# Performance work log

Measured on AMD Instinct MI355X. Metric: run time of the kernel, lower is better.

Reference implementation:

```python
import jax, jax.numpy as jnp
import numpy as np

I, O, R = 64, 64, 896          # input / output / regulatory protein counts
N = I + O + R                  # total GRN size
WARMUP = 25                    # warmup_count


def setup_inputs() -> dict:
    key = jax.random.key(0)
    k1, k2, k3, k4 = jax.random.split(key, 4)
    return {
        "inputs": jax.random.uniform(k1, (16384, I), dtype=jnp.float32),
        "identifiers": jax.random.uniform(k2, (N,), dtype=jnp.float32),
        "enhancers": jax.random.uniform(k3, (N,), dtype=jnp.float32),
        "inhibitors": jax.random.uniform(k4, (N,), dtype=jnp.float32),
        "beta": jnp.full((1,), 2.0, dtype=jnp.float32),
        "delta": jnp.full((1,), 1.0, dtype=jnp.float32),
    }


def _signatures(identifiers, enhancers, inhibitors, beta):
    # sig[j, i] = exp(-beta * |tag_j - id_i|): affinity of protein j regulating protein i.
    enh = jnp.exp(-beta * jnp.abs(enhancers[:, None] - identifiers[None, :]))
    inh = jnp.exp(-beta * jnp.abs(inhibitors[:, None] - identifiers[None, :]))
    # output proteins do not regulate others -> zero their rows
    mask = jnp.ones((N,), dtype=enh.dtype).at[I:I + O].set(0.0)[:, None]
    return enh * mask, inh * mask


def _step(conc, sig_diff, delta):
    # conc: [..., N]; sig_diff = enh_sigs - inh_sigs: [N, N]
    dc = (delta / N) * (conc @ sig_diff)
    new = jnp.maximum(conc + dc, 0.0)
    reg = new[..., I:]                                    # outputs + regulatory
    s = jnp.sum(reg, axis=-1, keepdims=True)
    reg = jnp.where(s > 0, reg / s, reg)                  # renormalize
    return jnp.concatenate([conc[..., :I], reg], axis=-1)  # inputs clamped


def reference(inputs, identifiers, enhancers, inhibitors, beta, delta):
    b, d = beta[0], delta[0]
    enh_s, inh_s = _signatures(identifiers, enhancers, inhibitors, b)
    sig_diff = enh_s - inh_s

    # setup(): uniform initial concentrations; warmup(): shared sequential steps
    conc0 = jnp.full((N,), 1.0 / N, dtype=jnp.float32)
    def warm(c, _):
        return _step(c, sig_diff, d), None
    conc, _ = jax.lax.scan(warm, conc0, None, length=WARMUP)

    # per-sample (batched instead of tf.map_fn): set input concs, one step
    B = inputs.shape[0]
    batch_conc = jnp.concatenate(
        [inputs, jnp.broadcast_to(conc[I:], (B, N - I))], axis=-1)
    new = _step(batch_conc, sig_diff, d)
    return new[..., I:I + O]  # output protein concentrations [B, O]
```

## Files before the change

### kernel.cpp

```cpp
#include <hip/hip_runtime.h>
#include <math.h>

#define NJ 960
#define NWARM 25
#define NFB 64
#define NC 15

typedef unsigned long long u64;
typedef unsigned int u32;

#define WK_F   4096u
#define BASE_F (WK_F + 64u * 960u)

__device__ __forceinline__ u64 pack_tv(u32 tag, float v) {
  return ((u64)tag << 32) | (u64)__float_as_uint(v);
}
__device__ __forceinline__ void ast(u64* p, u64 v) {
  __hip_atomic_store(p, v, __ATOMIC_RELAXED, __HIP_MEMORY_SCOPE_AGENT);
}
__device__ __forceinline__ u64 ald(const u64* p) {
  return __hip_atomic_load(p, __ATOMIC_RELAXED, __HIP_MEMORY_SCOPE_AGENT);
}

__global__ __launch_bounds__(1024) void front_k(const float* __restrict__ ident,
                                                const float* __restrict__ enh,
                                                const float* __restrict__ inh,
                                                const float* __restrict__ beta,
                                                const float* __restrict__ delta,
                                                void* __restrict__ wsv) {
  u64* Y = (u64*)wsv;
  u64* P = Y + 2 * NJ;
  float* Wk = (float*)wsv + WK_F;
  float* base = (float*)wsv + BASE_F;

  __shared__ float S2loc[NC * NJ];
  __shared__ float yloc[NJ];
  __shared__ float pvals[NFB];
  __shared__ float psums[NC];
  __shared__ float hdl[NC];

  const int tid = threadIdx.x;
  const int wid = tid >> 6, lane = tid & 63;
  const int b = blockIdx.x;
  const int j0 = b * NC;
  const float bc = beta[0];
  const float dN = delta[0] / 1024.0f;

  if (wid < NC) {
    int j = j0 + wid;
    float cj = ident[64 + j];
    float wv = dN * (expf(-bc * fabsf(enh[lane] - cj)) -
                     expf(-bc * fabsf(inh[lane] - cj)));
    Wk[(size_t)lane * NJ + j] = wv;
    float h = wv;
    #pragma unroll
    for (int off = 32; off >= 1; off >>= 1) h += __shfl_xor(h, off);
    if (lane == 0) hdl[wid] = h * (1.0f / 1024.0f);
  }
  for (int idx = tid; idx < NC * NJ; idx += 1024) {
    int c = idx / NJ, m = idx - c * NJ;
    float v = 0.0f;
    if (m >= 64) {
      float cj = ident[64 + j0 + c];
      int g = 64 + m;
      v = dN * (expf(-bc * fabsf(enh[g] - cj)) - expf(-bc * fabsf(inh[g] - cj)));
    }
    S2loc[idx] = v;
  }
  if (tid < NC) ast(&Y[j0 + tid], pack_tv(1u, 1.0f / 1024.0f));
  __syncthreads();

  for (int t = 0; t <= NWARM; ++t) {
    if (tid < NJ) {
      u64* src = &Y[(size_t)(t & 1) * NJ + tid];
      u64 v = ald(src);
      while ((u32)(v >> 32) != (u32)(t + 1)) {
        __builtin_amdgcn_s_sleep(1);
        v = ald(src);
      }
      yloc[tid] = __uint_as_float((u32)v);
    }
    if (t > 0 && tid < NFB) {
      u64* src = &P[(size_t)(t & 1) * NFB + tid];
      u64 v = ald(src);
      while ((u32)(v >> 32) != (u32)(t + 1)) {
        __builtin_amdgcn_s_sleep(1);
        v = ald(src);
      }
      pvals[tid] = __uint_as_float((u32)v);
    }
    __syncthreads();

    float s = 1.0f;
    if (t > 0) {
      float acc = 0.0f;
      #pragma unroll
      for (int i = 0; i < NFB; ++i) acc += pvals[i];
      s = acc;
    }

    if (wid < NC) {
      const float* __restrict__ row = &S2loc[wid * NJ];
      float d = 0.0f;
      #pragma unroll
      for (int i = 0; i < 15; ++i)
        d = fmaf(yloc[lane + 64 * i], row[lane + 64 * i], d);
      #pragma unroll
      for (int off = 32; off >= 1; off >>= 1) d += __shfl_xor(d, off);
      if (lane == 0) {
        float pre = yloc[j0 + wid] + d;
        pre = (s > 0.0f) ? pre / s : pre;
        if (t < NWARM) {
          float yv = fmaxf(pre + hdl[wid], 0.0f);
          psums[wid] = yv;
          ast(&Y[(size_t)((t + 1) & 1) * NJ + j0 + wid],
              pack_tv((u32)(t + 2), yv));
        } else {
          base[j0 + wid] = pre;
        }
      }
    }
    __syncthreads();

    if (t < NWARM && tid < NFB) {
      float pv = (tid < NC) ? psums[tid] : 0.0f;
      #pragma unroll
      for (int off = 32; off >= 1; off >>= 1) pv += __shfl_xor(pv, off);
      if (tid == 0)
        ast(&P[(size_t)((t + 1) & 1) * NFB + b], pack_tv((u32)(t + 2), pv));
    }
  }
}

__global__ __launch_bounds__(512) void batch_t(const float* __restrict__ inp,
                                               const float* __restrict__ ws,
                                               float* __restrict__ out) {
  __shared__ float At[64][66];
  __shared__ float Wl[16][516];
  __shared__ float bch[512];

  const int tid = threadIdx.x;
  const int colg = tid & 63;
  const int rowg = tid >> 6;
  const size_t rowbase = (size_t)blockIdx.x * 64;
  const float* __restrict__ Wk = ws + WK_F;
  const float* __restrict__ base = ws + BASE_F;

  #pragma unroll
  for (int i = 0; i < 2; ++i) {
    int fi = tid + i * 512;
    int r = fi >> 4, c4 = (fi & 15) * 4;
    float4 f4 = *(const float4*)(inp + (rowbase + r) * 64 + c4);
    At[c4 + 0][r] = f4.x; At[c4 + 1][r] = f4.y;
    At[c4 + 2][r] = f4.z; At[c4 + 3][r] = f4.w;
  }

  float rs[8];
  #pragma unroll
  for (int r = 0; r < 8; ++r) rs[r] = 0.0f;
  float acc[8][8];

  #pragma unroll 1
  for (int ch = 0; ch < 2; ++ch) {
    const int c0 = ch ? 0 : 512;
    #pragma unroll
    for (int r = 0; r < 8; ++r)
      #pragma unroll
      for (int c = 0; c < 8; ++c) acc[r][c] = 0.0f;

    __syncthreads();
    {
      int j = c0 + tid;
      bch[tid] = (j < 960) ? base[j] : -1.0e30f;
    }

    #pragma unroll 1
    for (int s = 0; s < 4; ++s) {
      __syncthreads();
      #pragma unroll
      for (int i = 0; i < 4; ++i) {
        int fi = tid + i * 512;
        int kk = fi >> 7;
        int c4 = (fi & 127) * 4;
        int j = c0 + c4;
        float4 v = make_float4(0.f, 0.f, 0.f, 0.f);
        if (j < 960)
          v = *(const float4*)(Wk + (size_t)(16 * s + kk) * NJ + j);
        *(float4*)&Wl[kk][c4] = v;
      }
      __syncthreads();

      #pragma unroll
      for (int kk = 0; kk < 16; ++kk) {
        float4 a0 = *(const float4*)&At[16 * s + kk][rowg * 8];
        float4 a1 = *(const float4*)&At[16 * s + kk][rowg * 8 + 4];
        float4 w0 = *(const float4*)&Wl[kk][colg * 8];
        float4 w1 = *(const float4*)&Wl[kk][colg * 8 + 4];
        float a[8] = {a0.x, a0.y, a0.z, a0.w, a1.x, a1.y, a1.z, a1.w};
        float w[8] = {w0.x, w0.y, w0.z, w0.w, w1.x, w1.y, w1.z, w1.w};
        #pragma unroll
        for (int r = 0; r < 8; ++r)
          #pragma unroll
          for (int c = 0; c < 8; ++c)
            acc[r][c] = fmaf(a[r], w[c], acc[r][c]);
      }
    }

    #pragma unroll
    for (int c = 0; c < 8; ++c) {
      float bv = bch[colg * 8 + c];
      #pragma unroll
      for (int r = 0; r < 8; ++r)
        rs[r] += fmaxf(acc[r][c] + bv, 0.0f);
    }
  }

  #pragma unroll
  for (int r = 0; r < 8; ++r) {
    float v = rs[r];
    #pragma unroll
    for (int off = 32; off >= 1; off >>= 1) v += __shfl_xor(v, off);
    rs[r] = v;
  }

  if (colg < 8) {
    #pragma unroll
    for (int r = 0; r < 8; ++r) {
      float inv = (rs[r] > 0.0f) ? 1.0f / rs[r] : 1.0f;
      float* op = out + (rowbase + rowg * 8 + r) * 64 + colg * 8;
      float4 o;
      o.x = fmaxf(acc[r][0] + bch[colg * 8 + 0], 0.0f) * inv;
      o.y = fmaxf(acc[r][1] + bch[colg * 8 + 1], 0.0f) * inv;
      o.z = fmaxf(acc[r][2] + bch[colg * 8 + 2], 0.0f) * inv;
      o.w = fmaxf(acc[r][3] + bch[colg * 8 + 3], 0.0f) * inv;
      *(float4*)op = o;
      o.x = fmaxf(acc[r][4] + bch[colg * 8 + 4], 0.0f) * inv;
      o.y = fmaxf(acc[r][5] + bch[colg * 8 + 5], 0.0f) * inv;
      o.z = fmaxf(acc[r][6] + bch[colg * 8 + 6], 0.0f) * inv;
      o.w = fmaxf(acc[r][7] + bch[colg * 8 + 7], 0.0f) * inv;
      *(float4*)(op + 4) = o;
    }
  }
}

extern "C" void kernel_launch(void* const* d_in, const int* in_sizes, int n_in,
                              void* d_out, int out_size, void* d_ws, size_t ws_size,
                              hipStream_t stream) {
  const float* inp   = (const float*)d_in[0];
  const float* ident = (const float*)d_in[1];
  const float* enh   = (const float*)d_in[2];
  const float* inh   = (const float*)d_in[3];
  const float* beta  = (const float*)d_in[4];
  const float* delta = (const float*)d_in[5];

  hipLaunchKernelGGL(front_k, dim3(NFB), dim3(1024), 0, stream,
                     ident, enh, inh, beta, delta, d_ws);
  hipLaunchKernelGGL(batch_t, dim3(256), dim3(512), 0, stream,
                     inp, (const float*)d_ws, (float*)d_out);
}
```

Baseline: 181.7 us.

## Replace warmup matvec with sorted prefix-sum evaluation of exp-abs kernel in one block

The warmup recurrence now runs in a single block. Each step's dense 960x896 matvec is replaced by an algebraic split: exp(-b|x-c|) factors into exp(±b x)·exp(∓b c), so the sums come from prefix scans over sources sorted by enhancer and inhibitor tags. Helper blocks compute the ranks, counts, the input-protein contributions and the W matrix, and publish them through tagged atomic flags. This removes the 64-block cross-block spin barriers on every step, at the cost of numerical risk from exp(b*x) products and a single-block serial chain.

```diff
diff --git a/kernel.cpp b/kernel.cpp
--- a/kernel.cpp
+++ b/kernel.cpp
@@ -2,133 +2,242 @@
 #include <math.h>
 
 #define NJ 960
+#define NSRC 896
 #define NWARM 25
-#define NFB 64
-#define NC 15
 
 typedef unsigned long long u64;
 typedef unsigned int u32;
 
-#define WK_F   4096u
+#define RK_O   0u
+#define CT_O   896u
+#define HD_O   1856u
+#define WK_F   8192u
 #define BASE_F (WK_F + 64u * 960u)
 
-__device__ __forceinline__ u64 pack_tv(u32 tag, float v) {
-  return ((u64)tag << 32) | (u64)__float_as_uint(v);
-}
+#define TAG_RK 0x524B0001u
+#define TAG_CT 0x43540001u
+#define TAG_HD 0x48440001u
+
 __device__ __forceinline__ void ast(u64* p, u64 v) {
   __hip_atomic_store(p, v, __ATOMIC_RELAXED, __HIP_MEMORY_SCOPE_AGENT);
 }
 __device__ __forceinline__ u64 ald(const u64* p) {
   return __hip_atomic_load(p, __ATOMIC_RELAXED, __HIP_MEMORY_SCOPE_AGENT);
 }
-
-__global__ __launch_bounds__(1024) void front_k(const float* __restrict__ ident,
-                                                const float* __restrict__ enh,
-                                                const float* __restrict__ inh,
-                                                const float* __restrict__ beta,
-                                                const float* __restrict__ delta,
-                                                void* __restrict__ wsv) {
-  u64* Y = (u64*)wsv;
-  u64* P = Y + 2 * NJ;
+__device__ __forceinline__ u32 poll32(const u64* p, u32 tag) {
+  u64 v = ald(p);
+  while ((u32)(v >> 32) != tag) { __builtin_amdgcn_s_sleep(1); v = ald(p); }
+  return (u32)v;
+}
+
+__global__ __launch_bounds__(256) void front_k(const float* __restrict__ ident,
+                                               const float* __restrict__ enh,
+                                               const float* __restrict__ inh,
+                                               const float* __restrict__ beta,
+                                               const float* __restrict__ delta,
+                                               void* __restrict__ wsv) {
+  u64* RK = (u64*)wsv + RK_O;
+  u64* CT = (u64*)wsv + CT_O;
+  u64* HD = (u64*)wsv + HD_O;
   float* Wk = (float*)wsv + WK_F;
   float* base = (float*)wsv + BASE_F;
 
-  __shared__ float S2loc[NC * NJ];
-  __shared__ float yloc[NJ];
-  __shared__ float pvals[NFB];
-  __shared__ float psums[NC];
-  __shared__ float hdl[NC];
-
   const int tid = threadIdx.x;
-  const int wid = tid >> 6, lane = tid & 63;
-  const int b = blockIdx.x;
-  const int j0 = b * NC;
-  const float bc = beta[0];
+  const float bb = beta[0];
   const float dN = delta[0] / 1024.0f;
 
-  if (wid < NC) {
-    int j = j0 + wid;
-    float cj = ident[64 + j];
-    float wv = dN * (expf(-bc * fabsf(enh[lane] - cj)) -
-                     expf(-bc * fabsf(inh[lane] - cj)));
-    Wk[(size_t)lane * NJ + j] = wv;
-    float h = wv;
-    #pragma unroll
-    for (int off = 32; off >= 1; off >>= 1) h += __shfl_xor(h, off);
-    if (lane == 0) hdl[wid] = h * (1.0f / 1024.0f);
-  }
-  for (int idx = tid; idx < NC * NJ; idx += 1024) {
-    int c = idx / NJ, m = idx - c * NJ;
-    float v = 0.0f;
-    if (m >= 64) {
-      float cj = ident[64 + j0 + c];
-      int g = 64 + m;
-      v = dN * (expf(-bc * fabsf(enh[g] - cj)) - expf(-bc * fabsf(inh[g] - cj)));
-    }
-    S2loc[idx] = v;
-  }
-  if (tid < NC) ast(&Y[j0 + tid], pack_tv(1u, 1.0f / 1024.0f));
+  if (blockIdx.x > 0) {
+    const int g = (blockIdx.x - 1) * 256 + tid;
+    const int c8 = g & 7;
+    if (g < NSRC * 8) {
+      int m = g >> 3;
+      float myE = enh[128 + m], myI = inh[128 + m];
+      int re = 0, ri = 0;
+      for (int i = 112 * c8; i < 112 * c8 + 112; ++i) {
+        float ev = enh[128 + i], iv = inh[128 + i];
+        re += (ev < myE || (ev == myE && i < m)) ? 1 : 0;
+        ri += (iv < myI || (iv == myI && i < m)) ? 1 : 0;
+      }
+      int p = re | (ri << 16);
+      p += __shfl_xor(p, 1); p += __shfl_xor(p, 2); p += __shfl_xor(p, 4);
+      if (c8 == 0) ast(&RK[m], ((u64)TAG_RK << 32) | (u32)p);
+    }
+    {
+      int j = g >> 3;
+      float cj = ident[64 + j];
+      int ce = 0, ci = 0;
+      for (int i = 112 * c8; i < 112 * c8 + 112; ++i) {
+        ce += (enh[128 + i] <= cj) ? 1 : 0;
+        ci += (inh[128 + i] <= cj) ? 1 : 0;
+      }
+      int p = ce | (ci << 16);
+      p += __shfl_xor(p, 1); p += __shfl_xor(p, 2); p += __shfl_xor(p, 4);
+      if (c8 == 0) ast(&CT[j], ((u64)TAG_CT << 32) | (u32)p);
+    }
+    {
+      int j = g >> 3;
+      float cj = ident[64 + j];
+      float h = 0.0f;
+      for (int k = 8 * c8; k < 8 * c8 + 8; ++k)
+        h += expf(-bb * fabsf(enh[k] - cj)) - expf(-bb * fabsf(inh[k] - cj));
+      h += __shfl_xor(h, 1); h += __shfl_xor(h, 2); h += __shfl_xor(h, 4);
+      if (c8 == 0)
+        ast(&HD[j], ((u64)TAG_HD << 32) |
+                    (u64)__float_as_uint(dN * h * (1.0f / 1024.0f)));
+    }
+    {
+      int k = g / 120;
+      int jb = (g % 120) * 8;
+      float ek = enh[k], ik = inh[k];
+      #pragma unroll
+      for (int u = 0; u < 8; ++u) {
+        float cj = ident[64 + jb + u];
+        Wk[(size_t)k * NJ + jb + u] =
+            dN * (expf(-bb * fabsf(ek - cj)) - expf(-bb * fabsf(ik - cj)));
+      }
+    }
+    return;
+  }
+
+  __shared__ float yl[NJ];
+  __shared__ float2 scanE[1024];
+  __shared__ float2 scanI[1024];
+  __shared__ float4 wtot[4];
+  __shared__ float ssw[4];
+
+  const int lane = tid & 63, wvid = tid >> 6;
+
+  int rE[4], rI[4];
+  if (tid < 224) {
+    #pragma unroll
+    for (int s = 0; s < 4; ++s) {
+      u32 v = poll32(&RK[4 * tid + s], TAG_RK);
+      rE[s] = v & 0xFFFF; rI[s] = v >> 16;
+    }
+  }
+  int cE[4], cI[4];
+  float hd[4], fm[4], fp[4];
+  if (tid < 240) {
+    #pragma unroll
+    for (int c = 0; c < 4; ++c) {
+      u32 v = poll32(&CT[4 * tid + c], TAG_CT);
+      cE[c] = v & 0xFFFF; cI[c] = v >> 16;
+      hd[c] = __uint_as_float(poll32(&HD[4 * tid + c], TAG_HD));
+      float cj = ident[64 + 4 * tid + c];
+      fm[c] = expf(-bb * cj); fp[c] = expf(bb * cj);
+    }
+  }
+  float EP[4], EN[4], IP[4], IN2[4];
+  if (tid < 224) {
+    #pragma unroll
+    for (int s = 0; s < 4; ++s) {
+      float e = enh[128 + 4 * tid + s], i2 = inh[128 + 4 * tid + s];
+      EP[s] = expf(bb * e);  EN[s] = expf(-bb * e);
+      IP[s] = expf(bb * i2); IN2[s] = expf(-bb * i2);
+    }
+  }
+  float y_own[4] = {1.0f / 1024.0f, 1.0f / 1024.0f, 1.0f / 1024.0f, 1.0f / 1024.0f};
+  if (tid < 240) {
+    #pragma unroll
+    for (int c = 0; c < 4; ++c) yl[4 * tid + c] = 1.0f / 1024.0f;
+  }
   __syncthreads();
 
   for (int t = 0; t <= NWARM; ++t) {
-    if (tid < NJ) {
-      u64* src = &Y[(size_t)(t & 1) * NJ + tid];
-      u64 v = ald(src);
-      while ((u32)(v >> 32) != (u32)(t + 1)) {
-        __builtin_amdgcn_s_sleep(1);
-        v = ald(src);
-      }
-      yloc[tid] = __uint_as_float((u32)v);
-    }
-    if (t > 0 && tid < NFB) {
-      u64* src = &P[(size_t)(t & 1) * NFB + tid];
-      u64 v = ald(src);
-      while ((u32)(v >> 32) != (u32)(t + 1)) {
-        __builtin_amdgcn_s_sleep(1);
-        v = ald(src);
-      }
-      pvals[tid] = __uint_as_float((u32)v);
-    }
-    __syncthreads();
-
-    float s = 1.0f;
-    if (t > 0) {
-      float acc = 0.0f;
-      #pragma unroll
-      for (int i = 0; i < NFB; ++i) acc += pvals[i];
-      s = acc;
-    }
-
-    if (wid < NC) {
-      const float* __restrict__ row = &S2loc[wid * NJ];
-      float d = 0.0f;
-      #pragma unroll
-      for (int i = 0; i < 15; ++i)
-        d = fmaf(yloc[lane + 64 * i], row[lane + 64 * i], d);
-      #pragma unroll
-      for (int off = 32; off >= 1; off >>= 1) d += __shfl_xor(d, off);
-      if (lane == 0) {
-        float pre = yloc[j0 + wid] + d;
-        pre = (s > 0.0f) ? pre / s : pre;
+    if (tid == 0) {
+      scanE[0] = make_float2(0.f, 0.f);
+      scanI[0] = make_float2(0.f, 0.f);
+    }
+    if (tid >= 224) {
+      #pragma unroll
+      for (int c = 0; c < 4; ++c) {
+        int p = 4 * tid + c;
+        if (p > NSRC) {
+          scanE[p] = make_float2(0.f, 0.f);
+          scanI[p] = make_float2(0.f, 0.f);
+        }
+      }
+    }
+    if (tid < 224) {
+      #pragma unroll
+      for (int s = 0; s < 4; ++s) {
+        float ym = yl[64 + 4 * tid + s];
+        scanE[rE[s] + 1] = make_float2(ym * EP[s], ym * EN[s]);
+        scanI[rI[s] + 1] = make_float2(ym * IP[s], ym * IN2[s]);
+      }
+    }
+    __syncthreads();
+
+    float2 e0 = scanE[4 * tid], e1 = scanE[4 * tid + 1],
+           e2 = scanE[4 * tid + 2], e3 = scanE[4 * tid + 3];
+    float2 i0 = scanI[4 * tid], i1 = scanI[4 * tid + 1],
+           i2v = scanI[4 * tid + 2], i3 = scanI[4 * tid + 3];
+    e1.x += e0.x; e1.y += e0.y; e2.x += e1.x; e2.y += e1.y; e3.x += e2.x; e3.y += e2.y;
+    i1.x += i0.x; i1.y += i0.y; i2v.x += i1.x; i2v.y += i1.y; i3.x += i2v.x; i3.y += i2v.y;
+    float4 tot = make_float4(e3.x, e3.y, i3.x, i3.y);
+    float4 inc = tot;
+    #pragma unroll
+    for (int off = 1; off < 64; off <<= 1) {
+      float ox = __shfl_up(inc.x, off, 64);
+      float oy = __shfl_up(inc.y, off, 64);
+      float oz = __shfl_up(inc.z, off, 64);
+      float ow = __shfl_up(inc.w, off, 64);
+      if (lane >= off) { inc.x += ox; inc.y += oy; inc.z += oz; inc.w += ow; }
+    }
+    if (lane == 63) wtot[wvid] = inc;
+    __syncthreads();
+    float4 exc = make_float4(inc.x - tot.x, inc.y - tot.y,
+                             inc.z - tot.z, inc.w - tot.w);
+    #pragma unroll
+    for (int w = 0; w < 3; ++w)
+      if (w < wvid) {
+        float4 p = wtot[w];
+        exc.x += p.x; exc.y += p.y; exc.z += p.z; exc.w += p.w;
+      }
+    e0.x += exc.x; e0.y += exc.y; e1.x += exc.x; e1.y += exc.y;
+    e2.x += exc.x; e2.y += exc.y; e3.x += exc.x; e3.y += exc.y;
+    i0.x += exc.z; i0.y += exc.w; i1.x += exc.z; i1.y += exc.w;
+    i2v.x += exc.z; i2v.y += exc.w; i3.x += exc.z; i3.y += exc.w;
+    scanE[4 * tid] = e0; scanE[4 * tid + 1] = e1;
+    scanE[4 * tid + 2] = e2; scanE[4 * tid + 3] = e3;
+    scanI[4 * tid] = i0; scanI[4 * tid + 1] = i1;
+    scanI[4 * tid + 2] = i2v; scanI[4 * tid + 3] = i3;
+    __syncthreads();
+
+    float nv[4] = {0.f, 0.f, 0.f, 0.f};
+    float psum = 0.0f;
+    if (tid < 240) {
+      float2 TE = scanE[NSRC], TI = scanI[NSRC];
+      #pragma unroll
+      for (int c = 0; c < 4; ++c) {
+        float2 AE = scanE[cE[c]], AI = scanI[cI[c]];
+        float dot = fm[c] * AE.x + fp[c] * (TE.y - AE.y)
+                  - fm[c] * AI.x - fp[c] * (TI.y - AI.y);
+        float pre = y_own[c] + dN * dot;
         if (t < NWARM) {
-          float yv = fmaxf(pre + hdl[wid], 0.0f);
-          psums[wid] = yv;
-          ast(&Y[(size_t)((t + 1) & 1) * NJ + j0 + wid],
-              pack_tv((u32)(t + 2), yv));
+          nv[c] = fmaxf(pre + hd[c], 0.0f);
+          psum += nv[c];
         } else {
-          base[j0 + wid] = pre;
+          base[4 * tid + c] = pre;
         }
       }
     }
-    __syncthreads();
-
-    if (t < NWARM && tid < NFB) {
-      float pv = (tid < NC) ? psums[tid] : 0.0f;
-      #pragma unroll
-      for (int off = 32; off >= 1; off >>= 1) pv += __shfl_xor(pv, off);
-      if (tid == 0)
-        ast(&P[(size_t)((t + 1) & 1) * NFB + b], pack_tv((u32)(t + 2), pv));
-    }
+    if (t < NWARM) {
+      #pragma unroll
+      for (int off = 32; off >= 1; off >>= 1) psum += __shfl_xor(psum, off);
+      if (lane == 0) ssw[wvid] = psum;
+      __syncthreads();
+      float s = ssw[0] + ssw[1] + ssw[2] + ssw[3];
+      float inv = (s > 0.0f) ? 1.0f / s : 1.0f;
+      if (tid < 240) {
+        #pragma unroll
+        for (int c = 0; c < 4; ++c) {
+          y_own[c] = nv[c] * inv;
+          yl[4 * tid + c] = y_own[c];
+        }
+      }
+    }
+    __syncthreads();
   }
 }
 
@@ -253,7 +362,7 @@
   const float* beta  = (const float*)d_in[4];
   const float* delta = (const float*)d_in[5];
 
-  hipLaunchKernelGGL(front_k, dim3(NFB), dim3(1024), 0, stream,
+  hipLaunchKernelGGL(front_k, dim3(31), dim3(256), 0, stream,
                      ident, enh, inh, beta, delta, d_ws);
   hipLaunchKernelGGL(batch_t, dim3(256), dim3(512), 0, stream,
                      inp, (const float*)d_ws, (float*)d_out);
```

New measurement: 158.8 us. 12.6% less time.
